# Kernel optimization log

Hardware: AMD Instinct MI355X
Metric: run time of the kernel (lower is better)

The kernel has to match this reference:

```python
import jax, jax.numpy as jnp
import numpy as np

ALPHA = 0.2  # LeakyReLU negative slope
NEG_BIG = -9e15


def setup_inputs() -> dict:
    key = jax.random.key(0)
    k1, k2, k3, k4 = jax.random.split(key, 4)
    N, F_in, F_out = 8192, 512, 256
    h = jax.random.normal(k1, (N, F_in), dtype=jnp.float32)
    adj = jax.random.randint(k2, (N, N), 0, 2, dtype=jnp.int32)
    # xavier_uniform with gain=1.414
    lim_W = 1.414 * np.sqrt(6.0 / (F_in + F_out))
    W = jax.random.uniform(k3, (F_in, F_out), jnp.float32, -lim_W, lim_W)
    lim_a = 1.414 * np.sqrt(6.0 / (2 * F_out + 1))
    a = jax.random.uniform(k4, (2 * F_out, 1), jnp.float32, -lim_a, lim_a)
    return {"h": h, "adj": adj, "W": W, "a": a}


def reference(h, adj, W, a):
    # Wh: [N, F_out]
    Wh = h @ W
    F_out = Wh.shape[1]
    # Decomposed score: e_ij = leakyrelu(a1.Wh_i + a2.Wh_j)
    f1 = Wh @ a[:F_out, 0]   # [N]
    f2 = Wh @ a[F_out:, 0]   # [N]
    e = f1[:, None] + f2[None, :]          # [N, N]
    e = jax.nn.leaky_relu(e, ALPHA)
    e = jnp.where(adj > 0, e, NEG_BIG)
    attention = jax.nn.softmax(e, axis=1)  # dropout omitted (eval mode)
    h_prime = attention @ Wh               # [N, F_out]
    return jax.nn.elu(h_prime)             # concat=True
```

## Files before the change

### kernel.cpp

```cpp
#include <hip/hip_runtime.h>
#include <hip/hip_bf16.h>
#include <cstdint>

#define NV 8192
#define FIN 512
#define FOUT 256
#define KS 4
#define ALPHA_LRELU 0.2f

using bf16x8 = __attribute__((ext_vector_type(8))) short;
using f32x4  = __attribute__((ext_vector_type(4))) float;

static __device__ __forceinline__ float b2f(ushort u) {
  union { uint32_t u32; float f; } v; v.u32 = ((uint32_t)u) << 16; return v.f;
}
static __device__ __forceinline__ ushort f2b(float f) {
  union { float f; uint32_t u; } v; v.f = f;
  uint32_t r = (v.u + 0x7fffu + ((v.u >> 16) & 1u)) >> 16;
  return (ushort)r;
}
static __device__ __forceinline__ uint32_t pk2(float a, float b) {
  return (uint32_t)f2b(a) | ((uint32_t)f2b(b) << 16);
}
static __device__ __forceinline__ int swz(int row, int kchunk) {
  return (row << 6) + (((kchunk ^ (row & 7)) & 7) << 3);
}
static __device__ __forceinline__ void gl_lds16(const ushort* g, ushort* l) {
  __builtin_amdgcn_global_load_lds(
      (const __attribute__((address_space(1))) uint32_t*)(uintptr_t)g,
      (__attribute__((address_space(3))) uint32_t*)(uint32_t)(uintptr_t)l,
      16, 0, 0);
}
#define SBAR0() __builtin_amdgcn_sched_barrier(0)

__global__ void k_prep_w(const float* __restrict__ W, ushort* __restrict__ WT,
                         float* __restrict__ f1z) {
  int t = blockIdx.x * 256 + threadIdx.x;
  int n = t >> 9, k = t & 511;
  WT[(size_t)n * FIN + k] = f2b(W[(size_t)k * FOUT + n]);
  if (t < 2 * NV) f1z[t] = 0.f;
}

__global__ __launch_bounds__(256, 2) void k_gemm1(
    const float* __restrict__ h, const ushort* __restrict__ WT,
    const float* __restrict__ a,
    ushort* __restrict__ WhT, float* __restrict__ f1, float* __restrict__ f2) {
  __shared__ __align__(16) ushort As[2][64 * 64];
  __shared__ __align__(16) ushort Ws[2][64 * 64];
  const int t = threadIdx.x;
  const int lane = t & 63;
  const int w = t >> 6;
  const int wm = w >> 1, wn = w & 1;
  const int i0 = blockIdx.x * 64;
  const int n0 = blockIdx.y * 64;
  const int srow = t & 63, sseg = t >> 6;
  const int NT1 = FIN / 64;

  f32x4 acc[2][2] = {};
  uint4 hA0, hA1, wA0, wA1;
  uint4 hB0, hB1, wB0, wB1;

  auto loadregs = [&](int kt, uint4& h0, uint4& h1, uint4& w0, uint4& w1) {
    const float4* gA = (const float4*)(h + (size_t)(i0 + srow) * FIN + kt * 64 + sseg * 16);
    float4 v0 = gA[0], v1 = gA[1], v2 = gA[2], v3 = gA[3];
    h0.x = pk2(v0.x, v0.y); h0.y = pk2(v0.z, v0.w);
    h0.z = pk2(v1.x, v1.y); h0.w = pk2(v1.z, v1.w);
    h1.x = pk2(v2.x, v2.y); h1.y = pk2(v2.z, v2.w);
    h1.z = pk2(v3.x, v3.y); h1.w = pk2(v3.z, v3.w);
    const uint4* gB = (const uint4*)(WT + (size_t)(n0 + srow) * FIN + kt * 64 + sseg * 16);
    w0 = gB[0]; w1 = gB[1];
  };
  auto writeLds = [&](const uint4& h0, const uint4& h1, const uint4& w0, const uint4& w1,
                      int buf) {
    *(uint4*)&As[buf][swz(srow, sseg * 2 + 0)] = h0;
    *(uint4*)&As[buf][swz(srow, sseg * 2 + 1)] = h1;
    *(uint4*)&Ws[buf][swz(srow, sseg * 2 + 0)] = w0;
    *(uint4*)&Ws[buf][swz(srow, sseg * 2 + 1)] = w1;
  };
  auto mfma1 = [&](int buf) {
#pragma unroll
    for (int kk = 0; kk < 2; ++kk) {
      const int kc = kk * 4 + (lane >> 4);
      bf16x8 af[2], bfv[2];
#pragma unroll
      for (int fi = 0; fi < 2; ++fi)
        af[fi] = *(const bf16x8*)&As[buf][swz(wm * 32 + fi * 16 + (lane & 15), kc)];
#pragma unroll
      for (int fj = 0; fj < 2; ++fj)
        bfv[fj] = *(const bf16x8*)&Ws[buf][swz(wn * 32 + fj * 16 + (lane & 15), kc)];
#pragma unroll
      for (int fi = 0; fi < 2; ++fi)
#pragma unroll
        for (int fj = 0; fj < 2; ++fj)
          acc[fi][fj] = __builtin_amdgcn_mfma_f32_16x16x32_bf16(af[fi], bfv[fj], acc[fi][fj], 0, 0, 0);
    }
  };

  loadregs(0, hA0, hA1, wA0, wA1);
  loadregs(1, hB0, hB1, wB0, wB1);
  writeLds(hA0, hA1, wA0, wA1, 0);
  __syncthreads();

  for (int kt = 0; kt + 2 < NT1; kt += 2) {
    loadregs(kt + 2, hA0, hA1, wA0, wA1);
    SBAR0();
    mfma1(0);
    writeLds(hB0, hB1, wB0, wB1, 1);
    __syncthreads();
    loadregs(kt + 3, hB0, hB1, wB0, wB1);
    SBAR0();
    mfma1(1);
    writeLds(hA0, hA1, wA0, wA1, 0);
    __syncthreads();
  }
  mfma1(0);
  writeLds(hB0, hB1, wB0, wB1, 1);
  __syncthreads();
  mfma1(1);

  float p1[2][4] = {}, p2[2][4] = {};
#pragma unroll
  for (int fi = 0; fi < 2; ++fi) {
    const int row0 = i0 + wm * 32 + fi * 16 + ((lane >> 4) << 2);
#pragma unroll
    for (int fj = 0; fj < 2; ++fj) {
      const int col = n0 + wn * 32 + fj * 16 + (lane & 15);
      const float a1c = a[col], a2c = a[FOUT + col];
      ushort ov[4];
      ushort4 o;
#pragma unroll
      for (int rr = 0; rr < 4; ++rr) {
        ov[rr] = f2b(acc[fi][fj][rr]);
        float v = b2f(ov[rr]);
        p1[fi][rr] = fmaf(v, a1c, p1[fi][rr]);
        p2[fi][rr] = fmaf(v, a2c, p2[fi][rr]);
      }
      o.x = ov[0]; o.y = ov[1]; o.z = ov[2]; o.w = ov[3];
      *(ushort4*)&WhT[(size_t)col * NV + row0] = o;
    }
  }
#pragma unroll
  for (int fi = 0; fi < 2; ++fi)
#pragma unroll
    for (int rr = 0; rr < 4; ++rr) {
      float s1 = p1[fi][rr], s2 = p2[fi][rr];
#pragma unroll
      for (int m = 1; m < 16; m <<= 1) {
        s1 += __shfl_xor(s1, m);
        s2 += __shfl_xor(s2, m);
      }
      if ((lane & 15) == 0) {
        const int row = i0 + wm * 32 + fi * 16 + ((lane >> 4) << 2) + rr;
        atomicAdd(&f1[row], s1);
        atomicAdd(&f2[row], s2);
      }
    }
}

__global__ __launch_bounds__(512, 4) void k_gemm2(
    const int* __restrict__ adj, const ushort* __restrict__ WhT,
    const float* __restrict__ f1, const float* __restrict__ f2,
    float* __restrict__ accP, float* __restrict__ Sp) {
  __shared__ __align__(16) ushort Ps[2][64 * 64];
  __shared__ __align__(16) ushort Bs[2][256 * 64];

  const int t = threadIdx.x;
  const int lane = t & 63;
  const int w = t >> 6;
  const int wm = w >> 2, wn = w & 3;
  const int bid = blockIdx.x;
  const int ks = bid & (KS - 1);
  const int rb = bid >> 2;
  const int i0 = rb * 64;
  const int jbase = ks * (NV / KS);
  const int NT = (NV / KS) / 64;

  const int pr = t >> 3, pq = t & 7;
  const float f1r = f1[i0 + pr];

  const int lrow = lane >> 3;
  const int lchunk = (lane & 7) ^ lrow;
  const ushort* wsrc0 = WhT + (size_t)(w * 32 + lrow) * NV + jbase + lchunk * 8;
  const int* adjp = adj + (size_t)(i0 + pr) * NV + jbase + pq * 8;
  const float* f2p = f2 + jbase + pq * 8;

  float ssum = 0.f;
  f32x4 acc[2][4] = {};
  int avA[8], avB[8];
  float fzA[8], fzB[8];

  auto adjload = [&](int tile, int (&av)[8]) {
    int4 a0 = *(const int4*)(adjp + tile * 64);
    int4 a1 = *(const int4*)(adjp + tile * 64 + 4);
    av[0] = a0.x; av[1] = a0.y; av[2] = a0.z; av[3] = a0.w;
    av[4] = a1.x; av[5] = a1.y; av[6] = a1.z; av[7] = a1.w;
  };
  auto fzload = [&](int tile, float (&fz)[8]) {
    float4 z0 = *(const float4*)(f2p + tile * 64);
    float4 z1 = *(const float4*)(f2p + tile * 64 + 4);
    fz[0] = z0.x; fz[1] = z0.y; fz[2] = z0.z; fz[3] = z0.w;
    fz[4] = z1.x; fz[5] = z1.y; fz[6] = z1.z; fz[7] = z1.w;
  };
  auto glB = [&](int tile, int buf) {
    const int koff = tile * 64;
#pragma unroll
    for (int q = 0; q < 4; ++q)
      gl_lds16(wsrc0 + (size_t)q * 8 * NV + koff, &Bs[buf][(w * 4 + q) * 512]);
  };
  auto finish = [&](const int (&av)[8], const float (&fz)[8], int buf) {
    ushort ub[8];
#pragma unroll
    for (int e = 0; e < 8; ++e) {
      float x = f1r + fz[e];
      float ee = fminf(fmaxf(x, ALPHA_LRELU * x), 75.f);
      float wv = (av[e] > 0) ? __expf(ee) : 0.f;
      ub[e] = f2b(wv);
      ssum += b2f(ub[e]);
    }
    uint4 pk;
    pk.x = (uint32_t)ub[0] | ((uint32_t)ub[1] << 16);
    pk.y = (uint32_t)ub[2] | ((uint32_t)ub[3] << 16);
    pk.z = (uint32_t)ub[4] | ((uint32_t)ub[5] << 16);
    pk.w = (uint32_t)ub[6] | ((uint32_t)ub[7] << 16);
    *(uint4*)&Ps[buf][swz(pr, pq)] = pk;
  };
  auto mfma_step = [&](int buf) {
#pragma unroll
    for (int kk = 0; kk < 2; ++kk) {
      const int kc = kk * 4 + (lane >> 4);
      bf16x8 af[2], bfv[4];
#pragma unroll
      for (int fi = 0; fi < 2; ++fi)
        af[fi] = *(const bf16x8*)&Ps[buf][swz(wm * 32 + fi * 16 + (lane & 15), kc)];
#pragma unroll
      for (int fj = 0; fj < 4; ++fj)
        bfv[fj] = *(const bf16x8*)&Bs[buf][swz(wn * 64 + fj * 16 + (lane & 15), kc)];
#pragma unroll
      for (int fi = 0; fi < 2; ++fi)
#pragma unroll
        for (int fj = 0; fj < 4; ++fj)
          acc[fi][fj] = __builtin_amdgcn_mfma_f32_16x16x32_bf16(af[fi], bfv[fj], acc[fi][fj], 0, 0, 0);
    }
  };

  glB(0, 0);
  adjload(0, avA); fzload(0, fzA);
  adjload(1, avB); fzload(1, fzB);
  SBAR0();
  finish(avA, fzA, 0);
  __syncthreads();

  for (int kt = 0; kt + 2 < NT; kt += 2) {
    glB(kt + 1, 1);
    adjload(kt + 2, avA); fzload(kt + 2, fzA);
    SBAR0();
    mfma_step(0);
    finish(avB, fzB, 1);
    __syncthreads();
    glB(kt + 2, 0);
    adjload(kt + 3, avB); fzload(kt + 3, fzB);
    SBAR0();
    mfma_step(1);
    finish(avA, fzA, 0);
    __syncthreads();
  }

  glB(NT - 1, 1);
  SBAR0();
  mfma_step(0);
  finish(avB, fzB, 1);
  __syncthreads();
  mfma_step(1);

  ssum += __shfl_xor(ssum, 1);
  ssum += __shfl_xor(ssum, 2);
  ssum += __shfl_xor(ssum, 4);
  if (pq == 0) Sp[(size_t)ks * NV + i0 + pr] = ssum;

  float* ab = accP + (size_t)ks * NV * FOUT;
#pragma unroll
  for (int fi = 0; fi < 2; ++fi) {
    const int ig = i0 + wm * 32 + fi * 16 + ((lane >> 4) << 2);
#pragma unroll
    for (int fj = 0; fj < 4; ++fj) {
      const int col = wn * 64 + fj * 16 + (lane & 15);
#pragma unroll
      for (int rr = 0; rr < 4; ++rr)
        ab[(size_t)(ig + rr) * FOUT + col] = acc[fi][fj][rr];
    }
  }
}

__global__ void k_combine(const float* __restrict__ accP, const float* __restrict__ Sp,
                          float* __restrict__ out) {
  const size_t NF = (size_t)NV * FOUT;
  int g = blockIdx.x * 256 + threadIdx.x;
  int i = g >> 6;
  float4 v0 = ((const float4*)accP)[g];
  float4 v1 = ((const float4*)(accP + NF))[g];
  float4 v2 = ((const float4*)(accP + 2 * NF))[g];
  float4 v3 = ((const float4*)(accP + 3 * NF))[g];
  float s = Sp[i] + Sp[NV + i] + Sp[2 * NV + i] + Sp[3 * NV + i];
  float inv = (s != 0.f) ? (1.0f / s) : 0.f;
  float xs0 = (v0.x + v1.x + v2.x + v3.x) * inv;
  float xs1 = (v0.y + v1.y + v2.y + v3.y) * inv;
  float xs2 = (v0.z + v1.z + v2.z + v3.z) * inv;
  float xs3 = (v0.w + v1.w + v2.w + v3.w) * inv;
  float4 o;
  o.x = xs0 > 0.f ? xs0 : expm1f(xs0);
  o.y = xs1 > 0.f ? xs1 : expm1f(xs1);
  o.z = xs2 > 0.f ? xs2 : expm1f(xs2);
  o.w = xs3 > 0.f ? xs3 : expm1f(xs3);
  ((float4*)out)[g] = o;
}

extern "C" void kernel_launch(void* const* d_in, const int* in_sizes, int n_in,
                              void* d_out, int out_size, void* d_ws, size_t ws_size,
                              hipStream_t stream) {
  const float* h   = (const float*)d_in[0];
  const int*   adj = (const int*)d_in[1];
  const float* W   = (const float*)d_in[2];
  const float* a   = (const float*)d_in[3];
  float* out = (float*)d_out;

  char* ws = (char*)d_ws;
  ushort* WT   = (ushort*)ws;
  ushort* WhT  = (ushort*)(ws + (256ull << 10));
  float*  f1   = (float*)(ws + (256ull << 10) + (4ull << 20));
  float*  f2   = f1 + NV;
  float*  Sp   = f2 + NV;
  float*  accP = Sp + (size_t)KS * NV;

  k_prep_w<<<(FIN * FOUT) / 256, 256, 0, stream>>>(W, WT, f1);
  k_gemm1<<<dim3(NV / 64, FOUT / 64), 256, 0, stream>>>(h, WT, a, WhT, f1, f2);
  k_gemm2<<<(NV / 64) * KS, 512, 0, stream>>>(adj, WhT, f1, f2, accP, Sp);
  k_combine<<<(NV * FOUT / 4) / 256, 256, 0, stream>>>(accP, Sp, out);
}
```

Before: 423.6 us.

## Halve k-tile to 32, split-K into 8 parts, raise occupancy to 8 blocks

```diff
diff --git a/kernel.cpp b/kernel.cpp
--- a/kernel.cpp
+++ b/kernel.cpp
@@ -5,7 +5,7 @@
 #define NV 8192
 #define FIN 512
 #define FOUT 256
-#define KS 4
+#define KS 8
 #define ALPHA_LRELU 0.2f
 
 using bf16x8 = __attribute__((ext_vector_type(8))) short;
@@ -157,12 +157,12 @@
     }
 }
 
-__global__ __launch_bounds__(512, 4) void k_gemm2(
+__global__ __launch_bounds__(512, 8) void k_gemm2(
     const int* __restrict__ adj, const ushort* __restrict__ WhT,
     const float* __restrict__ f1, const float* __restrict__ f2,
     float* __restrict__ accP, float* __restrict__ Sp) {
-  __shared__ __align__(16) ushort Ps[2][64 * 64];
-  __shared__ __align__(16) ushort Bs[2][256 * 64];
+  __shared__ __align__(16) ushort Ps[2][64 * 32];
+  __shared__ __align__(16) ushort Bs[2][256 * 32];
 
   const int t = threadIdx.x;
   const int lane = t & 63;
@@ -170,107 +170,83 @@
   const int wm = w >> 2, wn = w & 3;
   const int bid = blockIdx.x;
   const int ks = bid & (KS - 1);
-  const int rb = bid >> 2;
+  const int rb = bid >> 3;
   const int i0 = rb * 64;
   const int jbase = ks * (NV / KS);
-  const int NT = (NV / KS) / 64;
+  const int NT = (NV / KS) / 32;
 
   const int pr = t >> 3, pq = t & 7;
   const float f1r = f1[i0 + pr];
 
-  const int lrow = lane >> 3;
-  const int lchunk = (lane & 7) ^ lrow;
+  const int lrow = lane >> 2;
+  const int lchunk = (lane & 3) ^ (lrow & 3);
   const ushort* wsrc0 = WhT + (size_t)(w * 32 + lrow) * NV + jbase + lchunk * 8;
-  const int* adjp = adj + (size_t)(i0 + pr) * NV + jbase + pq * 8;
-  const float* f2p = f2 + jbase + pq * 8;
+  const int* adjp = adj + (size_t)(i0 + pr) * NV + jbase + pq * 4;
+  const float* f2p = f2 + jbase + pq * 4;
+  const int koff = ((lane >> 4) ^ (lane & 3)) * 8;
 
   float ssum = 0.f;
   f32x4 acc[2][4] = {};
-  int avA[8], avB[8];
-  float fzA[8], fzB[8];
-
-  auto adjload = [&](int tile, int (&av)[8]) {
-    int4 a0 = *(const int4*)(adjp + tile * 64);
-    int4 a1 = *(const int4*)(adjp + tile * 64 + 4);
+  int av[4]; float fz[4];
+
+  auto adjload = [&](int tile) {
+    int4 a0 = *(const int4*)(adjp + tile * 32);
     av[0] = a0.x; av[1] = a0.y; av[2] = a0.z; av[3] = a0.w;
-    av[4] = a1.x; av[5] = a1.y; av[6] = a1.z; av[7] = a1.w;
-  };
-  auto fzload = [&](int tile, float (&fz)[8]) {
-    float4 z0 = *(const float4*)(f2p + tile * 64);
-    float4 z1 = *(const float4*)(f2p + tile * 64 + 4);
+  };
+  auto fzload = [&](int tile) {
+    float4 z0 = *(const float4*)(f2p + tile * 32);
     fz[0] = z0.x; fz[1] = z0.y; fz[2] = z0.z; fz[3] = z0.w;
-    fz[4] = z1.x; fz[5] = z1.y; fz[6] = z1.z; fz[7] = z1.w;
   };
   auto glB = [&](int tile, int buf) {
-    const int koff = tile * 64;
-#pragma unroll
-    for (int q = 0; q < 4; ++q)
-      gl_lds16(wsrc0 + (size_t)q * 8 * NV + koff, &Bs[buf][(w * 4 + q) * 512]);
-  };
-  auto finish = [&](const int (&av)[8], const float (&fz)[8], int buf) {
-    ushort ub[8];
-#pragma unroll
-    for (int e = 0; e < 8; ++e) {
+#pragma unroll
+    for (int q = 0; q < 2; ++q)
+      gl_lds16(wsrc0 + (size_t)q * 16 * NV + tile * 32, &Bs[buf][w * 1024 + q * 512]);
+  };
+  auto finish = [&](int buf) {
+    ushort ub[4];
+#pragma unroll
+    for (int e = 0; e < 4; ++e) {
       float x = f1r + fz[e];
       float ee = fminf(fmaxf(x, ALPHA_LRELU * x), 75.f);
       float wv = (av[e] > 0) ? __expf(ee) : 0.f;
       ub[e] = f2b(wv);
       ssum += b2f(ub[e]);
     }
-    uint4 pk;
+    uint2 pk;
     pk.x = (uint32_t)ub[0] | ((uint32_t)ub[1] << 16);
     pk.y = (uint32_t)ub[2] | ((uint32_t)ub[3] << 16);
-    pk.z = (uint32_t)ub[4] | ((uint32_t)ub[5] << 16);
-    pk.w = (uint32_t)ub[6] | ((uint32_t)ub[7] << 16);
-    *(uint4*)&Ps[buf][swz(pr, pq)] = pk;
+    const int off = pr * 32 + (((pq >> 1) ^ (pr & 3)) & 3) * 8 + (pq & 1) * 4;
+    *(uint2*)&Ps[buf][off] = pk;
   };
   auto mfma_step = [&](int buf) {
-#pragma unroll
-    for (int kk = 0; kk < 2; ++kk) {
-      const int kc = kk * 4 + (lane >> 4);
-      bf16x8 af[2], bfv[4];
-#pragma unroll
-      for (int fi = 0; fi < 2; ++fi)
-        af[fi] = *(const bf16x8*)&Ps[buf][swz(wm * 32 + fi * 16 + (lane & 15), kc)];
+    bf16x8 af[2], bfv[4];
+#pragma unroll
+    for (int fi = 0; fi < 2; ++fi)
+      af[fi] = *(const bf16x8*)&Ps[buf][(wm * 32 + fi * 16 + (lane & 15)) * 32 + koff];
+#pragma unroll
+    for (int fj = 0; fj < 4; ++fj)
+      bfv[fj] = *(const bf16x8*)&Bs[buf][(wn * 64 + fj * 16 + (lane & 15)) * 32 + koff];
+#pragma unroll
+    for (int fi = 0; fi < 2; ++fi)
 #pragma unroll
       for (int fj = 0; fj < 4; ++fj)
-        bfv[fj] = *(const bf16x8*)&Bs[buf][swz(wn * 64 + fj * 16 + (lane & 15), kc)];
-#pragma unroll
-      for (int fi = 0; fi < 2; ++fi)
-#pragma unroll
-        for (int fj = 0; fj < 4; ++fj)
-          acc[fi][fj] = __builtin_amdgcn_mfma_f32_16x16x32_bf16(af[fi], bfv[fj], acc[fi][fj], 0, 0, 0);
-    }
-  };
-
+        acc[fi][fj] = __builtin_amdgcn_mfma_f32_16x16x32_bf16(af[fi], bfv[fj], acc[fi][fj], 0, 0, 0);
+  };
+
+  adjload(0); fzload(0);
   glB(0, 0);
-  adjload(0, avA); fzload(0, fzA);
-  adjload(1, avB); fzload(1, fzB);
-  SBAR0();
-  finish(avA, fzA, 0);
+  finish(0);
   __syncthreads();
 
-  for (int kt = 0; kt + 2 < NT; kt += 2) {
-    glB(kt + 1, 1);
-    adjload(kt + 2, avA); fzload(kt + 2, fzA);
+  for (int p = 0; p + 1 < NT; ++p) {
+    adjload(p + 1); fzload(p + 1);
+    glB(p + 1, (p + 1) & 1);
     SBAR0();
-    mfma_step(0);
-    finish(avB, fzB, 1);
+    mfma_step(p & 1);
+    finish((p + 1) & 1);
     __syncthreads();
-    glB(kt + 2, 0);
-    adjload(kt + 3, avB); fzload(kt + 3, fzB);
-    SBAR0();
-    mfma_step(1);
-    finish(avA, fzA, 0);
-    __syncthreads();
-  }
-
-  glB(NT - 1, 1);
-  SBAR0();
-  mfma_step(0);
-  finish(avB, fzB, 1);
-  __syncthreads();
-  mfma_step(1);
+  }
+  mfma_step((NT - 1) & 1);
 
   ssum += __shfl_xor(ssum, 1);
   ssum += __shfl_xor(ssum, 2);
@@ -296,16 +272,16 @@
   const size_t NF = (size_t)NV * FOUT;
   int g = blockIdx.x * 256 + threadIdx.x;
   int i = g >> 6;
-  float4 v0 = ((const float4*)accP)[g];
-  float4 v1 = ((const float4*)(accP + NF))[g];
-  float4 v2 = ((const float4*)(accP + 2 * NF))[g];
-  float4 v3 = ((const float4*)(accP + 3 * NF))[g];
-  float s = Sp[i] + Sp[NV + i] + Sp[2 * NV + i] + Sp[3 * NV + i];
+  float4 vs = {0.f, 0.f, 0.f, 0.f};
+  float s = 0.f;
+#pragma unroll
+  for (int p = 0; p < KS; ++p) {
+    float4 v = ((const float4*)(accP + (size_t)p * NF))[g];
+    vs.x += v.x; vs.y += v.y; vs.z += v.z; vs.w += v.w;
+    s += Sp[(size_t)p * NV + i];
+  }
   float inv = (s != 0.f) ? (1.0f / s) : 0.f;
-  float xs0 = (v0.x + v1.x + v2.x + v3.x) * inv;
-  float xs1 = (v0.y + v1.y + v2.y + v3.y) * inv;
-  float xs2 = (v0.z + v1.z + v2.z + v3.z) * inv;
-  float xs3 = (v0.w + v1.w + v2.w + v3.w) * inv;
+  float xs0 = vs.x * inv, xs1 = vs.y * inv, xs2 = vs.z * inv, xs3 = vs.w * inv;
   float4 o;
   o.x = xs0 > 0.f ? xs0 : expm1f(xs0);
   o.y = xs1 > 0.f ? xs1 : expm1f(xs1);
```

After: 515.0 us. 1.22x slower.
